# Kernel optimization log

Measured on AMD Instinct MI355X. Metric: run time of the kernel, lower is better.

## Reference

```python
import jax, jax.numpy as jnp
import numpy as np

KS = 2        # kernel_size
DIL = 1       # dilation
FILTERS = 512
Z_DIM = 128
B, C, T = 8, 512, 4096
TZ = T + 2 * (KS - 1)


def _conv1d(x, w, b):
    # x: (B, L, Cin), w: (ks, Cin, Cout) -> VALID conv, channels-last (keras Conv1D)
    y = jax.lax.conv_general_dilated(x, w, window_strides=(1,), padding='VALID',
                                     dimension_numbers=('NWC', 'WIO', 'NWC'))
    return y + b


def _adaptor(z, w1, b1, w2, b2):
    return _conv1d(jax.nn.relu(_conv1d(z, w1, b1)), w2, b2)


def setup_inputs() -> dict:
    key = jax.random.key(0)
    ks = jax.random.split(key, 10)
    lim = np.sqrt(6.0 / FILTERS)
    u = lambda k, shp: jax.random.uniform(k, shp, jnp.float32, -lim, lim)
    return {
        'x': jax.random.normal(ks[0], (B, C, T), jnp.float32),
        'z': jax.random.normal(ks[1], (B, TZ, Z_DIM), jnp.float32),
        'ww1': u(ks[2], (KS, Z_DIM, FILTERS)), 'wb1': jnp.zeros((FILTERS,), jnp.float32),
        'ww2': u(ks[3], (KS, FILTERS, FILTERS)), 'wb2': jnp.zeros((FILTERS,), jnp.float32),
        'bw1': u(ks[4], (KS, Z_DIM, FILTERS)), 'bb1': jnp.zeros((FILTERS,), jnp.float32),
        'bw2': u(ks[5], (KS, FILTERS, FILTERS)), 'bb2': jnp.zeros((FILTERS,), jnp.float32),
    }


def reference(x, z, ww1, wb1, ww2, wb2, bw1, bb1, bw2, bb2):
    m = x.shape[1]
    t = x.shape[2]
    pad = DIL * (KS - 1)
    xp = jnp.pad(x, ((0, 0), (0, 0), (0, pad)))
    end = t + pad
    # im2col-style unfold: (B, C*KS, T)
    xu = jnp.concatenate([xp[:, :, pad - i * DIL: end - i * DIL] for i in range(KS)], axis=1)
    weights = _adaptor(z, ww1, wb1, ww2, wb2)   # (B, T, F)
    bias = _adaptor(z, bw1, bb1, bw2, bb2)      # (B, T, F)
    y = jnp.matmul(xu, weights)                 # (B, C*KS, F)
    return y[:, :m, :] + bias[:, :m, :]
```

## Files before the change

kernel.cpp:

```cpp
#include <hip/hip_runtime.h>

typedef short short8 __attribute__((ext_vector_type(8)));
typedef float float4v __attribute__((ext_vector_type(4)));
typedef __attribute__((address_space(1))) const unsigned int gu32;
typedef __attribute__((address_space(3))) unsigned int lu32;

__device__ __forceinline__ unsigned short f2bf(float f) {
  unsigned int u = __builtin_bit_cast(unsigned int, f);
  u += 0x7FFFu + ((u >> 16) & 1u);
  return (unsigned short)(u >> 16);
}
__device__ __forceinline__ float bf2f(unsigned short s) {
  return __builtin_bit_cast(float, (unsigned int)s << 16);
}

template<int N> __device__ __forceinline__ void vmwait() {
  if constexpr (N == 0) asm volatile("s_waitcnt vmcnt(0)" ::: "memory");
  else if constexpr (N == 2) asm volatile("s_waitcnt vmcnt(2)" ::: "memory");
  else if constexpr (N == 3) asm volatile("s_waitcnt vmcnt(3)" ::: "memory");
  else if constexpr (N == 4) asm volatile("s_waitcnt vmcnt(4)" ::: "memory");
  else if constexpr (N == 6) asm volatile("s_waitcnt vmcnt(6)" ::: "memory");
  else if constexpr (N == 8) asm volatile("s_waitcnt vmcnt(8)" ::: "memory");
  else if constexpr (N == 9) asm volatile("s_waitcnt vmcnt(9)" ::: "memory");
  else if constexpr (N == 12) asm volatile("s_waitcnt vmcnt(12)" ::: "memory");
}

__device__ __forceinline__ int rswz(int r) { return (r & 3) ^ ((r >> 2) & 3); }

__global__ __launch_bounds__(256) void prep(
    const float* __restrict__ ww1, const float* __restrict__ ww2,
    const float* __restrict__ bw1, const float* __restrict__ bw2,
    const float* __restrict__ z, const float* __restrict__ x,
    unsigned short* __restrict__ w1T, unsigned short* __restrict__ w2T,
    unsigned short* __restrict__ b1T, unsigned short* __restrict__ b2T,
    unsigned short* __restrict__ zb,
    unsigned short* __restrict__ xs, unsigned short* __restrict__ xz,
    float* __restrict__ rs)
{
  __shared__ float lds[64][65];
  const int b = blockIdx.x;
  const int tid = threadIdx.x;
  if (b < 320) {
    const float* src; unsigned short* dst; int K, tile;
    if (b < 32)       { src = ww1; dst = w1T; K = 256;  tile = b; }
    else if (b < 160) { src = ww2; dst = w2T; K = 1024; tile = b - 32; }
    else if (b < 192) { src = bw1; dst = b1T; K = 256;  tile = b - 160; }
    else              { src = bw2; dst = b2T; K = 1024; tile = b - 192; }
    int ntk = K >> 6;
    int k0 = (tile % ntk) * 64, n0 = (tile / ntk) * 64;
    int nl = tid & 63, kh = tid >> 6;
#pragma unroll
    for (int p = 0; p < 16; ++p)
      lds[kh * 16 + p][nl] = src[(long long)(k0 + kh * 16 + p) * 512 + n0 + nl];
    __syncthreads();
    int nr = tid >> 2, q = tid & 3;
    unsigned short tmp[16];
#pragma unroll
    for (int u = 0; u < 16; ++u) tmp[u] = f2bf(lds[q * 16 + u][nr]);
    unsigned short* op = dst + (long long)(n0 + nr) * K + k0 + q * 16;
    *(uint4*)op = *(uint4*)tmp;
    *(uint4*)(op + 8) = *(uint4*)(tmp + 8);
  } else if (b < 1345) {
    long long base = (long long)(b - 320) * 4096 + tid * 16;
    if (base < 4196352) {
      const float4* zp = (const float4*)(z + base);
      unsigned int pk[8];
#pragma unroll
      for (int q2 = 0; q2 < 4; ++q2) {
        float4 f = zp[q2];
        pk[q2 * 2]     = (unsigned int)f2bf(f.x) | ((unsigned int)f2bf(f.y) << 16);
        pk[q2 * 2 + 1] = (unsigned int)f2bf(f.z) | ((unsigned int)f2bf(f.w) << 16);
      }
      *(uint4*)(zb + base)     = *(uint4*)pk;
      *(uint4*)(zb + base + 8) = *(uint4*)(pk + 4);
    }
  } else {
    float* red = &lds[0][0];
    long long r = b - 1345;
    const float* xr = x + r * 4096;
    int t0 = tid * 16;
    float v[17];
    const float4* xr4 = (const float4*)(xr + t0);
#pragma unroll
    for (int q = 0; q < 4; ++q) {
      float4 f = xr4[q];
      v[q * 4] = f.x; v[q * 4 + 1] = f.y; v[q * 4 + 2] = f.z; v[q * 4 + 3] = f.w;
    }
    v[16] = (t0 + 16 < 4096) ? xr[t0 + 16] : 0.f;
    unsigned int spk[8], zpk[8];
    float sum = 0.f;
#pragma unroll
    for (int q = 0; q < 8; ++q) {
      unsigned short s0 = f2bf(v[2 * q + 1]);
      unsigned short s1 = f2bf(v[2 * q + 2]);
      sum += bf2f(s0);
      sum += bf2f(s1);
      spk[q] = (unsigned int)s0 | ((unsigned int)s1 << 16);
      unsigned short z0 = (t0 == 0 && q == 0) ? (unsigned short)0 : f2bf(v[2 * q]);
      unsigned short z1 = f2bf(v[2 * q + 1]);
      zpk[q] = (unsigned int)z0 | ((unsigned int)z1 << 16);
    }
    *(uint4*)(xs + r * 4096 + t0)     = *(uint4*)(spk);
    *(uint4*)(xs + r * 4096 + t0 + 8) = *(uint4*)(spk + 4);
    *(uint4*)(xz + r * 4096 + t0)     = *(uint4*)(zpk);
    *(uint4*)(xz + r * 4096 + t0 + 8) = *(uint4*)(zpk + 4);
#pragma unroll
    for (int off = 32; off > 0; off >>= 1) sum += __shfl_down(sum, off);
    if ((tid & 63) == 0) red[tid >> 6] = sum;
    __syncthreads();
    if (tid == 0) rs[r] = red[0] + red[1] + red[2] + red[3];
  }
}

template<int BM, int BN, bool RELU, bool OBF16, bool TRANS, bool SPLITK, int NH,
         bool ROWPACK, int NREG>
__device__ __forceinline__ void gemm_core(
    int bx, int by, int bz, int nzTot, unsigned short* smem,
    const unsigned short* __restrict__ A,
    const unsigned short* __restrict__ A2,
    const unsigned short* __restrict__ Bt,
    const float* __restrict__ biasv,
    void* __restrict__ outp,
    void* __restrict__ outp2,
    int M, int Kchunk, int RPB, int EXTRA, int BSCALE,
    int nHalf, int bRowMask,
    long long bStrideB, long long outBatchStride, int outLd)
{
  constexpr int WM = BM / 2, WN = BN / 2;
  constexpr int NI = WM / 16, NJ = WN / 16;
  constexpr int AI = BM / 64;
  constexpr int BI = BN / 64;
  constexpr int SA1 = BM * 32, SB1 = BN * 32;
  unsigned short* sB0 = smem + (NREG > 0 ? 1 : NH) * SA1;

  const int tid  = threadIdx.x;
  const int lane = tid & 63;
  const int wave = tid >> 6;
  const int wm = wave >> 1, wn = wave & 1;
  const int lr = lane & 15, quad = lane >> 4;

  const int r0 = bx * BM;
  const int n0 = by * BN;
  const int bb = r0 / RPB;
  const int Ktot = SPLITK ? Kchunk * nzTot : Kchunk;
  const int kOff = SPLITK ? bz * Kchunk : 0;
  const long long bOffB = (long long)bb * bStrideB;
  const unsigned short* Ae = (nHalf && n0 >= nHalf) ? A2 : A;

  const int srow = lane >> 2;
  const int sg = (lane & 3) ^ rswz(srow);
  const unsigned short* gA[AI];
#pragma unroll
  for (int c = 0; c < AI; ++c) {
    int instr = c * 4 + wave;
    int row = instr * 16 + srow;
    int r = r0 + row; if (r > M - 1) r = M - 1;
    gA[c] = Ae + ((long long)r + (long long)(r / RPB) * EXTRA) * BSCALE + kOff + sg * 8;
  }
  const unsigned short* gB[BI];
#pragma unroll
  for (int c = 0; c < BI; ++c) {
    int instr = c * 4 + wave;
    int row = instr * 16 + srow;
    gB[c] = Bt + (long long)((n0 + row) & bRowMask) * Ktot + bOffB + kOff + sg * 8;
  }

  int aoff[NI], boff[NJ];
#pragma unroll
  for (int i = 0; i < NI; ++i) {
    int rr = wm * WM + i * 16 + lr;
    aoff[i] = rr * 32 + ((quad ^ rswz(rr)) * 8);
  }
#pragma unroll
  for (int j = 0; j < NJ; ++j) {
    int rr = wn * WN + j * 16 + lr;
    boff[j] = rr * 32 + ((quad ^ rswz(rr)) * 8);
  }

  float4v acc[NI][NJ];
  const float4v z4 = {0.f, 0.f, 0.f, 0.f};
#pragma unroll
  for (int i = 0; i < NI; ++i)
#pragma unroll
    for (int j = 0; j < NJ; ++j) acc[i][j] = z4;

  if constexpr (NREG > 0) {
    constexpr int RS = SA1 + SB1;
    const int NT = Kchunk >> 5;
    auto stg = [&](int t, int m) {
      unsigned short* rb = smem + m * RS;
      int kk = t * 32;
#pragma unroll
      for (int c = 0; c < AI; ++c)
        __builtin_amdgcn_global_load_lds((gu32*)(gA[c] + kk),
                                         (lu32*)(rb + (c * 4 + wave) * 512), 16, 0, 0);
#pragma unroll
      for (int c = 0; c < BI; ++c)
        __builtin_amdgcn_global_load_lds((gu32*)(gB[c] + kk),
                                         (lu32*)(rb + SA1 + (c * 4 + wave) * 512), 16, 0, 0);
    };
#pragma unroll
    for (int i = 0; i < NREG - 1; ++i) if (i < NT) stg(i, i);
    int m = 0;
    for (int t = 0; t < NT; ++t) {
      const int ahead = NT - 1 - t;
      if (ahead >= NREG - 2)      vmwait<(NREG - 2) * (AI + BI)>();
      else if (ahead == 2)        vmwait<2 * (AI + BI)>();
      else if (ahead == 1)        vmwait<AI + BI>();
      else                        vmwait<0>();
      __builtin_amdgcn_s_barrier();
      __builtin_amdgcn_sched_barrier(0);
      int m2 = m + NREG - 1; if (m2 >= NREG) m2 -= NREG;
      if (t + NREG - 1 < NT) stg(t + NREG - 1, m2);
      const unsigned short* rb = smem + m * RS;
      short8 af[NI], bfr[NJ];
#pragma unroll
      for (int i = 0; i < NI; ++i) af[i] = *(const short8*)(rb + aoff[i]);
#pragma unroll
      for (int j = 0; j < NJ; ++j) bfr[j] = *(const short8*)(rb + SA1 + boff[j]);
#pragma unroll
      for (int i = 0; i < NI; ++i)
#pragma unroll
        for (int j = 0; j < NJ; ++j)
          acc[i][j] = __builtin_amdgcn_mfma_f32_16x16x32_bf16(af[i], bfr[j], acc[i][j], 0, 0, 0);
      if (++m == NREG) m = 0;
    }
    __syncthreads();
  } else {
    for (int k0 = 0; k0 < Kchunk; k0 += 32 * NH) {
#pragma unroll
      for (int h = 0; h < NH; ++h) {
#pragma unroll
        for (int c = 0; c < AI; ++c)
          __builtin_amdgcn_global_load_lds((gu32*)(gA[c] + k0 + h * 32),
                                           (lu32*)(smem + (c * 4 + wave) * 512 + h * SA1), 16, 0, 0);
#pragma unroll
        for (int c = 0; c < BI; ++c)
          __builtin_amdgcn_global_load_lds((gu32*)(gB[c] + k0 + h * 32),
                                           (lu32*)(sB0 + (c * 4 + wave) * 512 + h * SB1), 16, 0, 0);
      }
      __syncthreads();
#pragma unroll
      for (int h = 0; h < NH; ++h) {
        short8 af[NI], bfr[NJ];
#pragma unroll
        for (int i = 0; i < NI; ++i) af[i] = *(const short8*)(smem + h * SA1 + aoff[i]);
#pragma unroll
        for (int j = 0; j < NJ; ++j) bfr[j] = *(const short8*)(sB0 + h * SB1 + boff[j]);
#pragma unroll
        for (int i = 0; i < NI; ++i)
#pragma unroll
          for (int j = 0; j < NJ; ++j)
            acc[i][j] = __builtin_amdgcn_mfma_f32_16x16x32_bf16(af[i], bfr[j], acc[i][j], 0, 0, 0);
      }
      __syncthreads();
    }
  }

  if (TRANS) {
    unsigned short* Ts = smem;
    const int t0l = r0 - bb * RPB;
#pragma unroll
    for (int p = 0; p < 2; ++p) {
      if (wn == p) {
#pragma unroll
        for (int j = 0; j < NJ; ++j) {
          int frl = j * 16 + lr;
          float bv = biasv[n0 + p * WN + frl];
#pragma unroll
          for (int i = 0; i < NI; ++i) {
            int tr = wm * WM + i * 16 + quad * 4;
            unsigned long long pk = 0;
#pragma unroll
            for (int g = 0; g < 4; ++g) {
              float vv = acc[i][j][g] + bv;
              if (RELU) vv = fmaxf(vv, 0.f);
              pk |= (unsigned long long)f2bf(vv) << (16 * g);
            }
            *(unsigned long long*)(Ts + frl * (BM + 8) + tr) = pk;
          }
        }
      }
      __syncthreads();
      int frl = tid >> 2, sgg = tid & 3;
      unsigned short* dst = (unsigned short*)outp + (long long)bb * outBatchStride
                          + (long long)(n0 + p * WN + frl) * outLd + t0l + sgg * (BM / 4);
      const unsigned short* srcp = Ts + frl * (BM + 8) + sgg * (BM / 4);
#pragma unroll
      for (int u = 0; u < BM / 32; ++u)
        *(uint4*)(dst + u * 8) = *(const uint4*)(srcp + u * 8);
      __syncthreads();
    }
  } else if (ROWPACK) {
    constexpr int P  = (BM > 64) ? 2 : 1;
    constexpr int RP = BM / P;
    constexpr int BNP = BN + 8;
    constexpr int TPR = 256 / RP;
    constexpr int EPT = BN / TPR;
    void* op = (SPLITK && bz) ? outp2 : outp;
    unsigned short* R = smem;
#pragma unroll
    for (int p = 0; p < P; ++p) {
      if (P == 1 || wm == p) {
#pragma unroll
        for (int j = 0; j < NJ; ++j) {
          int cc = wn * WN + j * 16 + lr;
#pragma unroll
          for (int i = 0; i < NI; ++i) {
            int rl = (P == 1 ? wm * WM : 0) + i * 16 + quad * 4;
#pragma unroll
            for (int g = 0; g < 4; ++g)
              R[(rl + g) * BNP + cc] = f2bf(acc[i][j][g]);
          }
        }
      }
      __syncthreads();
      int rloc = tid / TPR, part = tid % TPR;
      unsigned short* dstp = (unsigned short*)op
                           + (long long)(r0 + p * RP + rloc) * outLd + n0 + part * EPT;
      const unsigned short* srcp = R + rloc * BNP + part * EPT;
#pragma unroll
      for (int u = 0; u < EPT / 8; ++u)
        *(uint4*)(dstp + u * 8) = *(const uint4*)(srcp + u * 8);
      if (p + 1 < P) __syncthreads();
    }
  } else {
    void* op = (SPLITK && bz) ? outp2 : outp;
#pragma unroll
    for (int j = 0; j < NJ; ++j) {
      int n_g = n0 + wn * WN + j * 16 + lr;
      float bv = biasv ? biasv[n_g] : 0.f;
#pragma unroll
      for (int i = 0; i < NI; ++i) {
        int r_base = r0 + wm * WM + i * 16 + quad * 4;
#pragma unroll
        for (int g = 0; g < 4; ++g) {
          int r_g = r_base + g;
          if (r_g >= M) continue;
          float v = acc[i][j][g] + bv;
          if (RELU) v = fmaxf(v, 0.f);
          long long oidx = (long long)r_g * outLd + n_g;
          if (OBF16) ((unsigned short*)op)[oidx] = f2bf(v);
          else       ((float*)op)[oidx] = v;
        }
      }
    }
  }
}

template<int BM, int BN, bool RELU, bool OBF16, bool TRANS, bool SPLITK, int NH,
         bool ROWPACK, int NREG, bool REMAP>
__global__ __launch_bounds__(256)
void gemm_bt(const unsigned short* __restrict__ A,
             const unsigned short* __restrict__ A2,
             const unsigned short* __restrict__ Bt,
             const float* __restrict__ biasv,
             void* __restrict__ outp,
             void* __restrict__ outp2,
             int M, int Kchunk, int RPB, int EXTRA, int BSCALE,
             int nHalf, int bRowMask,
             long long bStrideB, long long outBatchStride, int outLd)
{
  constexpr int STAGE = (NREG > 0 ? NREG : NH) * (BM * 32 + BN * 32);
  constexpr int REPK = TRANS ? (BN / 2) * (BM + 8)
                     : (ROWPACK ? (BM > 64 ? (BM / 2) * (BN + 8) : BM * (BN + 8)) : 0);
  constexpr int SMEMN = (REPK > STAGE) ? REPK : STAGE;
  __shared__ unsigned short smem[SMEMN];
  int bx, by, bz, nz;
  if (REMAP) {
    int lin = blockIdx.x;
    bx = (lin & 7) * 4 + ((lin >> 3) & 3);
    by = (lin >> 5) & 7;
    bz = lin >> 8;
    nz = 2;
  } else {
    bx = blockIdx.x; by = blockIdx.y; bz = blockIdx.z; nz = gridDim.z;
  }
  gemm_core<BM, BN, RELU, OBF16, TRANS, SPLITK, NH, ROWPACK, NREG>(
      bx, by, bz, nz, smem,
      A, A2, Bt, biasv, outp, outp2,
      M, Kchunk, RPB, EXTRA, BSCALE, nHalf, bRowMask,
      bStrideB, outBatchStride, outLd);
}

__global__ __launch_bounds__(256) void conv1(
    const unsigned short* __restrict__ zb,
    const unsigned short* __restrict__ w1T,
    const unsigned short* __restrict__ b1T,
    const float* __restrict__ wb1,
    const float* __restrict__ bb1,
    unsigned short* __restrict__ h1T,
    unsigned short* __restrict__ h1b)
{
  __shared__ unsigned short smem[24576];
  int g = blockIdx.x;
  if (g < 1024) {
    gemm_core<128, 128, true, true, true, false, 1, false, 3>(
        g & 255, g >> 8, 0, 1, smem,
        zb, nullptr, w1T, wb1, h1T, nullptr,
        32768, 256, 4096, 2, 128, 0, 0xFFFF, 0, 512ll * 4096, 4096);
  } else {
    int idx = g - 1024;
    gemm_core<64, 128, true, true, false, false, 1, false, 3>(
        idx % 65, idx / 65, 0, 1, smem,
        zb, nullptr, b1T, bb1, h1b, nullptr,
        4104, 256, 513, 3585, 128, 0, 0xFFFF, 0, 0, 512);
  }
}

__global__ __launch_bounds__(256) void final_gemm3(
    const unsigned short* __restrict__ p0,
    const unsigned short* __restrict__ p1,
    const unsigned short* __restrict__ h1b,
    const unsigned short* __restrict__ w2T,
    const unsigned short* __restrict__ b2T,
    const float* __restrict__ rs,
    const float* __restrict__ wb2,
    const float* __restrict__ bb2,
    float* __restrict__ out)
{
  constexpr int RS = 8192;
  __shared__ unsigned short smem[4 * RS];
  const int tid = threadIdx.x;
  const int lane = tid & 63, wave = tid >> 6;
  const int wm = wave >> 1, wn = wave & 1;
  const int lr = lane & 15, quad = lane >> 4;
  const int r0 = blockIdx.x * 64, n0 = blockIdx.y * 64;

  const int srow = lane >> 2;
  const int sg = (lane & 3) ^ rswz(srow);
  const int row = wave * 16 + srow;
  const int rA = r0 + row;
  const int rB = n0 + row;
  const unsigned short* aP[3] = {
    p0 + (long long)rA * 1024 + sg * 8,
    p1 + (long long)rA * 1024 + sg * 8,
    h1b + ((long long)rA + (rA >> 9)) * 512 + sg * 8 };
  const unsigned short* bP[3] = {
    w2T + (long long)rB * 1024 + sg * 8,
    w2T + (long long)rB * 1024 + sg * 8,
    b2T + (long long)rB * 1024 + sg * 8 };

  int aoff[2], boff[2];
#pragma unroll
  for (int i = 0; i < 2; ++i) {
    int rr = wm * 32 + i * 16 + lr;
    aoff[i] = rr * 32 + ((quad ^ rswz(rr)) * 8);
    int nn = wn * 32 + i * 16 + lr;
    boff[i] = nn * 32 + ((quad ^ rswz(nn)) * 8);
  }

  float4v acc[2][2];
  const float4v z4 = {0.f, 0.f, 0.f, 0.f};
  acc[0][0] = z4; acc[0][1] = z4; acc[1][0] = z4; acc[1][1] = z4;

  const int wslot = wave * 512;
  auto stg = [&](int t, int m) {
    int k = t * 64; int seg = k >> 10; int kk = k & 1023;
    unsigned short* base = smem + m * RS;
    __builtin_amdgcn_global_load_lds((gu32*)(aP[seg] + kk),      (lu32*)(base + wslot), 16, 0, 0);
    __builtin_amdgcn_global_load_lds((gu32*)(aP[seg] + kk + 32), (lu32*)(base + 2048 + wslot), 16, 0, 0);
    __builtin_amdgcn_global_load_lds((gu32*)(bP[seg] + kk),      (lu32*)(base + 4096 + wslot), 16, 0, 0);
    __builtin_amdgcn_global_load_lds((gu32*)(bP[seg] + kk + 32), (lu32*)(base + 6144 + wslot), 16, 0, 0);
  };
  stg(0, 0); stg(1, 1); stg(2, 2);
  int m = 0;
  for (int t = 0; t < 48; ++t) {
    if (t <= 45)      vmwait<8>();
    else if (t == 46) vmwait<4>();
    else              vmwait<0>();
    __builtin_amdgcn_s_barrier();
    __builtin_amdgcn_sched_barrier(0);
    int m2 = m + 3; if (m2 >= 4) m2 -= 4;
    if (t + 3 < 48) stg(t + 3, m2);
    const unsigned short* base = smem + m * RS;
#pragma unroll
    for (int h = 0; h < 2; ++h) {
      short8 af[2], bfr[2];
      af[0] = *(const short8*)(base + h * 2048 + aoff[0]);
      af[1] = *(const short8*)(base + h * 2048 + aoff[1]);
      bfr[0] = *(const short8*)(base + 4096 + h * 2048 + boff[0]);
      bfr[1] = *(const short8*)(base + 4096 + h * 2048 + boff[1]);
#pragma unroll
      for (int i = 0; i < 2; ++i)
#pragma unroll
        for (int j = 0; j < 2; ++j)
          acc[i][j] = __builtin_amdgcn_mfma_f32_16x16x32_bf16(af[i], bfr[j], acc[i][j], 0, 0, 0);
    }
    if (++m == 4) m = 0;
  }

#pragma unroll
  for (int j = 0; j < 2; ++j) {
    int n_g = n0 + wn * 32 + j * 16 + lr;
    float w2b = wb2[n_g], bbv = bb2[n_g];
#pragma unroll
    for (int i = 0; i < 2; ++i) {
      int rb2 = r0 + wm * 32 + i * 16 + quad * 4;
#pragma unroll
      for (int g = 0; g < 4; ++g) {
        int r_g = rb2 + g;
        out[(long long)r_g * 512 + n_g] = acc[i][j][g] + rs[r_g] * w2b + bbv;
      }
    }
  }
}

extern "C" void kernel_launch(void* const* d_in, const int* in_sizes, int n_in,
                              void* d_out, int out_size, void* d_ws, size_t ws_size,
                              hipStream_t stream) {
  const float* x   = (const float*)d_in[0];
  const float* z   = (const float*)d_in[1];
  const float* ww1 = (const float*)d_in[2];
  const float* wb1 = (const float*)d_in[3];
  const float* ww2 = (const float*)d_in[4];
  const float* wb2 = (const float*)d_in[5];
  const float* bw1 = (const float*)d_in[6];
  const float* bb1 = (const float*)d_in[7];
  const float* bw2 = (const float*)d_in[8];
  const float* bb2 = (const float*)d_in[9];

  char* ws = (char*)d_ws;
  unsigned short* xs  = (unsigned short*)ws; ws += 16777216ll * 2;
  unsigned short* xz  = (unsigned short*)ws; ws += 16777216ll * 2;
  unsigned short* zb  = (unsigned short*)ws; ws += 4196352ll  * 2;
  unsigned short* h1T = (unsigned short*)ws; ws += 16777216ll * 2;
  unsigned short* h1b = (unsigned short*)ws; ws += 2101248ll  * 2;
  unsigned short* w2T = (unsigned short*)ws; ws += 524288ll * 2;
  unsigned short* b2T = (unsigned short*)ws; ws += 524288ll * 2;
  float* rs = (float*)ws;                    ws += 4096ll * 4;
  char* tail = ws;
  unsigned short* w1T = (unsigned short*)tail;
  unsigned short* b1T = (unsigned short*)tail + 131072;
  unsigned short* p0  = zb;
  unsigned short* p1  = (unsigned short*)tail;

  prep<<<5441, 256, 0, stream>>>(ww1, ww2, bw1, bw2, z, x,
                                 w1T, w2T, b1T, b2T, zb, xs, xz, rs);
  conv1<<<1284, 256, 0, stream>>>(zb, w1T, b1T, wb1, bb1, h1T, h1b);
  gemm_bt<128, 128, false, true, false, true, 1, true, 5, true><<<512, 256, 0, stream>>>(
      xs, xz, h1T, nullptr, p0, p1,
      4096, 2048, 512, 0, 4096, 512, 511, 512ll * 4096, 0, 1024);
  final_gemm3<<<dim3(64, 8), 256, 0, stream>>>(
      p0, p1, h1b, w2T, b2T, rs, wb2, bb2, (float*)d_out);
}
```

Baseline: 230.3 us.

## Replace generic split-K GEMM with dedicated 256x128 tile, 512-thread kernel

Swaps the templated gemm_bt launch (128x128 tiles, 256 threads, 512 blocks) for a specialised gemm_G kernel using 256x128 tiles with 8 waves and 256 blocks. It keeps a 5-slot LDS ring with 4-stage prefetch via global_load_lds and writes bf16 results through an LDS staging buffer so global stores are coalesced 16-byte writes. The larger tile raises reuse of the B operand and cuts per-block overhead. In exchange it uses more LDS per block and launches fewer blocks, which could leave CUs idle on a 256-CU device.

```diff
diff --git a/kernel.cpp b/kernel.cpp
--- a/kernel.cpp
+++ b/kernel.cpp
@@ -348,41 +348,6 @@
   }
 }
 
-template<int BM, int BN, bool RELU, bool OBF16, bool TRANS, bool SPLITK, int NH,
-         bool ROWPACK, int NREG, bool REMAP>
-__global__ __launch_bounds__(256)
-void gemm_bt(const unsigned short* __restrict__ A,
-             const unsigned short* __restrict__ A2,
-             const unsigned short* __restrict__ Bt,
-             const float* __restrict__ biasv,
-             void* __restrict__ outp,
-             void* __restrict__ outp2,
-             int M, int Kchunk, int RPB, int EXTRA, int BSCALE,
-             int nHalf, int bRowMask,
-             long long bStrideB, long long outBatchStride, int outLd)
-{
-  constexpr int STAGE = (NREG > 0 ? NREG : NH) * (BM * 32 + BN * 32);
-  constexpr int REPK = TRANS ? (BN / 2) * (BM + 8)
-                     : (ROWPACK ? (BM > 64 ? (BM / 2) * (BN + 8) : BM * (BN + 8)) : 0);
-  constexpr int SMEMN = (REPK > STAGE) ? REPK : STAGE;
-  __shared__ unsigned short smem[SMEMN];
-  int bx, by, bz, nz;
-  if (REMAP) {
-    int lin = blockIdx.x;
-    bx = (lin & 7) * 4 + ((lin >> 3) & 3);
-    by = (lin >> 5) & 7;
-    bz = lin >> 8;
-    nz = 2;
-  } else {
-    bx = blockIdx.x; by = blockIdx.y; bz = blockIdx.z; nz = gridDim.z;
-  }
-  gemm_core<BM, BN, RELU, OBF16, TRANS, SPLITK, NH, ROWPACK, NREG>(
-      bx, by, bz, nz, smem,
-      A, A2, Bt, biasv, outp, outp2,
-      M, Kchunk, RPB, EXTRA, BSCALE, nHalf, bRowMask,
-      bStrideB, outBatchStride, outLd);
-}
-
 __global__ __launch_bounds__(256) void conv1(
     const unsigned short* __restrict__ zb,
     const unsigned short* __restrict__ w1T,
@@ -408,6 +373,119 @@
   }
 }
 
+__global__ __launch_bounds__(512) void gemm_G(
+    const unsigned short* __restrict__ xs,
+    const unsigned short* __restrict__ xz,
+    const unsigned short* __restrict__ h1T,
+    unsigned short* __restrict__ p0,
+    unsigned short* __restrict__ p1)
+{
+  constexpr int SA = 8192;
+  constexpr int RS = SA + 4096;
+  __shared__ unsigned short smem[5 * RS];
+  const int tid = threadIdx.x;
+  const int lane = tid & 63, wave = tid >> 6;
+  const int wm = wave >> 1, wn = wave & 1;
+  const int lr = lane & 15, quad = lane >> 4;
+
+  const int lin = blockIdx.x;
+  const int bx = (lin & 7) * 2 + ((lin >> 3) & 1);
+  const int by = (lin >> 4) & 7;
+  const int bz = lin >> 7;
+  const int r0 = bx * 256, n0 = by * 128;
+  const int bb = r0 >> 9;
+  const int kOff = bz * 2048;
+  const unsigned short* Ae = (n0 >= 512) ? xz : xs;
+
+  const int srow = lane >> 2;
+  const int sg = (lane & 3) ^ rswz(srow);
+  const unsigned short* gA[2];
+#pragma unroll
+  for (int c = 0; c < 2; ++c) {
+    int r = r0 + (c * 8 + wave) * 16 + srow;
+    gA[c] = Ae + (long long)r * 4096 + kOff + sg * 8;
+  }
+  const unsigned short* gB =
+      h1T + (long long)((n0 + wave * 16 + srow) & 511) * 4096
+          + (long long)bb * (512ll * 4096) + kOff + sg * 8;
+
+  int aoff[4], boff[4];
+#pragma unroll
+  for (int i = 0; i < 4; ++i) {
+    int rr = wm * 64 + i * 16 + lr;
+    aoff[i] = rr * 32 + ((quad ^ rswz(rr)) * 8);
+    int nn = wn * 64 + i * 16 + lr;
+    boff[i] = SA + nn * 32 + ((quad ^ rswz(nn)) * 8);
+  }
+
+  float4v acc[4][4];
+  const float4v z4 = {0.f, 0.f, 0.f, 0.f};
+#pragma unroll
+  for (int i = 0; i < 4; ++i)
+#pragma unroll
+    for (int j = 0; j < 4; ++j) acc[i][j] = z4;
+
+  auto stg = [&](int t, int m) {
+    unsigned short* rb = smem + m * RS;
+    int kk = t * 32;
+    __builtin_amdgcn_global_load_lds((gu32*)(gA[0] + kk), (lu32*)(rb + wave * 512), 16, 0, 0);
+    __builtin_amdgcn_global_load_lds((gu32*)(gA[1] + kk), (lu32*)(rb + (8 + wave) * 512), 16, 0, 0);
+    __builtin_amdgcn_global_load_lds((gu32*)(gB + kk),    (lu32*)(rb + SA + wave * 512), 16, 0, 0);
+  };
+  stg(0, 0); stg(1, 1); stg(2, 2); stg(3, 3);
+  int m = 0;
+  for (int t = 0; t < 64; ++t) {
+    const int ahead = 63 - t;
+    if (ahead >= 3)      vmwait<9>();
+    else if (ahead == 2) vmwait<6>();
+    else if (ahead == 1) vmwait<3>();
+    else                 vmwait<0>();
+    __builtin_amdgcn_s_barrier();
+    __builtin_amdgcn_sched_barrier(0);
+    int m2 = m + 4; if (m2 >= 5) m2 -= 5;
+    if (t + 4 < 64) stg(t + 4, m2);
+    const unsigned short* rb = smem + m * RS;
+    short8 af[4], bfr[4];
+#pragma unroll
+    for (int i = 0; i < 4; ++i) af[i] = *(const short8*)(rb + aoff[i]);
+#pragma unroll
+    for (int j = 0; j < 4; ++j) bfr[j] = *(const short8*)(rb + boff[j]);
+#pragma unroll
+    for (int i = 0; i < 4; ++i)
+#pragma unroll
+      for (int j = 0; j < 4; ++j)
+        acc[i][j] = __builtin_amdgcn_mfma_f32_16x16x32_bf16(af[i], bfr[j], acc[i][j], 0, 0, 0);
+    if (++m == 5) m = 0;
+  }
+  __syncthreads();
+
+  unsigned short* op = bz ? p1 : p0;
+  unsigned short* R = smem;
+#pragma unroll
+  for (int p = 0; p < 4; ++p) {
+    if (wm == p) {
+#pragma unroll
+      for (int j = 0; j < 4; ++j) {
+        int cc = wn * 64 + j * 16 + lr;
+#pragma unroll
+        for (int i = 0; i < 4; ++i) {
+          int rl = i * 16 + quad * 4;
+#pragma unroll
+          for (int g = 0; g < 4; ++g)
+            R[(rl + g) * 136 + cc] = f2bf(acc[i][j][g]);
+        }
+      }
+    }
+    __syncthreads();
+    int rloc = tid >> 3, part = tid & 7;
+    unsigned short* dstp = op + (long long)(r0 + p * 64 + rloc) * 1024 + n0 + part * 16;
+    const unsigned short* srcp = R + rloc * 136 + part * 16;
+    *(uint4*)dstp       = *(const uint4*)srcp;
+    *(uint4*)(dstp + 8) = *(const uint4*)(srcp + 8);
+    if (p + 1 < 4) __syncthreads();
+  }
+}
+
 __global__ __launch_bounds__(256) void final_gemm3(
     const unsigned short* __restrict__ p0,
     const unsigned short* __restrict__ p1,
@@ -538,9 +616,7 @@
   prep<<<5441, 256, 0, stream>>>(ww1, ww2, bw1, bw2, z, x,
                                  w1T, w2T, b1T, b2T, zb, xs, xz, rs);
   conv1<<<1284, 256, 0, stream>>>(zb, w1T, b1T, wb1, bb1, h1T, h1b);
-  gemm_bt<128, 128, false, true, false, true, 1, true, 5, true><<<512, 256, 0, stream>>>(
-      xs, xz, h1T, nullptr, p0, p1,
-      4096, 2048, 512, 0, 4096, 512, 511, 512ll * 4096, 0, 1024);
+  gemm_G<<<256, 512, 0, stream>>>(xs, xz, h1T, p0, p1);
   final_gemm3<<<dim3(64, 8), 256, 0, stream>>>(
       p0, p1, h1b, w2T, b2T, rs, wb2, bb2, (float*)d_out);
 }
```

Result: no change. 230.0 us (-0.1%).
